# Performance work log

Measured on AMD Instinct MI355X. Metric: run time of the kernel, lower is better.

Reference implementation:

```python
import jax, jax.numpy as jnp
import numpy as np

N, IN_DIM, HID, HEADS, HOPS, NCLS, E = 20000, 1536, 256, 4, 3, 3, 320000
HD = HID // HEADS
EPS = 1e-5
NEG_SLOPE = 0.2


def layer_norm(x, g, b):
    mu = jnp.mean(x, axis=-1, keepdims=True)
    var = jnp.var(x, axis=-1, keepdims=True)
    return (x - mu) * jax.lax.rsqrt(var + EPS) * g + b


def gatv2(x, src, dst, Wl, bl, Wr, br, att, bias):
    # x: [N, HID]; src/dst: [E'] (self loops included)
    xl = (x @ Wl + bl).reshape(N, HEADS, HD)  # source transform
    xr = (x @ Wr + br).reshape(N, HEADS, HD)  # target transform
    e = jax.nn.leaky_relu(xl[src] + xr[dst], NEG_SLOPE)          # [E', H, D]
    logits = jnp.einsum('ehd,hd->eh', e, att)                     # [E', H]
    m = jax.ops.segment_max(logits, dst, num_segments=N)         # [N, H]
    ex = jnp.exp(logits - m[dst])
    denom = jax.ops.segment_sum(ex, dst, num_segments=N)
    alpha = ex / denom[dst]                                       # softmax per dst
    msg = xl[src] * alpha[:, :, None]                             # [E', H, D]
    out = jax.ops.segment_sum(msg, dst, num_segments=N)
    return out.reshape(N, HID) + bias


def setup_inputs() -> dict:
    key = jax.random.key(0)
    ks = jax.random.split(key, 20)
    s = lambda k, shp, sc: jax.random.normal(k, shp, jnp.float32) * sc
    return {
        'features': s(ks[0], (N, IN_DIM), 1.0),
        'edge_index': jax.random.randint(ks[1], (2, E), 0, N, jnp.int64),
        'proj_W': s(ks[2], (IN_DIM, HID), 0.02),
        'proj_b': jnp.zeros((HID,), jnp.float32),
        'n0_g': jnp.ones((HID,), jnp.float32),
        'n0_b': jnp.zeros((HID,), jnp.float32),
        'Wl': s(ks[3], (HOPS, HID, HID), 0.05),
        'bl': jnp.zeros((HOPS, HID), jnp.float32),
        'Wr': s(ks[4], (HOPS, HID, HID), 0.05),
        'br': jnp.zeros((HOPS, HID), jnp.float32),
        'att': s(ks[5], (HOPS, HEADS, HD), 0.1),
        'gbias': jnp.zeros((HOPS, HID), jnp.float32),
        'ln_g': jnp.ones((HOPS, HID), jnp.float32),
        'ln_b': jnp.zeros((HOPS, HID), jnp.float32),
        'h1_W': s(ks[6], (HID, HID), 0.05),
        'h1_b': jnp.zeros((HID,), jnp.float32),
        'h2_W': s(ks[7], (HID, NCLS), 0.05),
        'h2_b': jnp.zeros((NCLS,), jnp.float32),
    }


def reference(features, edge_index, proj_W, proj_b, n0_g, n0_b, Wl, bl, Wr, br,
              att, gbias, ln_g, ln_b, h1_W, h1_b, h2_W, h2_b):
    # add self loops (PyG GATv2Conv default)
    loop = jnp.arange(N, dtype=edge_index.dtype)
    src = jnp.concatenate([edge_index[0], loop])
    dst = jnp.concatenate([edge_index[1], loop])

    x = layer_norm(features @ proj_W + proj_b, n0_g, n0_b)
    for h in range(HOPS):
        g = gatv2(x, src, dst, Wl[h], bl[h], Wr[h], br[h], att[h], gbias[h])
        x = layer_norm(g + x, ln_g[h], ln_b[h])
    # head (dropout inactive at eval); torch GELU is exact erf form
    x = jax.nn.gelu(x @ h1_W + h1_b, approximate=False)
    return x @ h2_W + h2_b
```

## Files before the change

### kernel.cpp

```cpp
#include <hip/hip_runtime.h>
#include <hip/hip_bf16.h>
#include <math.h>

#define NN 20000
#define INDIM 1536
#define HID 256
#define NE 320000
#define NEDGE (NE + NN)
#define EPSV 1e-5f
#define NEG 0.2f

typedef unsigned short ushort_b;
typedef unsigned int uint32;
typedef __bf16 bf16x8 __attribute__((ext_vector_type(8)));
typedef float f32x4 __attribute__((ext_vector_type(4)));

#define AS1(p) ((const __attribute__((address_space(1))) void*)(p))
#define AS3(p) ((__attribute__((address_space(3))) void*)(p))

__device__ inline ushort_b f2bf(float x) {
  union { float f; uint32 u; } v; v.f = x;
  uint32 r = v.u + 0x7FFFu + ((v.u >> 16) & 1u);
  return (ushort_b)(r >> 16);
}
__device__ inline float bf2f(ushort_b h) {
  union { uint32 u; float f; } v; v.u = ((uint32)h) << 16;
  return v.f;
}
__device__ inline float4 ldbf4(const ushort_b* p) {
  ushort4 u = *(const ushort4*)p;
  float4 f;
  f.x = bf2f(u.x); f.y = bf2f(u.y); f.z = bf2f(u.z); f.w = bf2f(u.w);
  return f;
}

template<int OUTMODE>
__global__ __launch_bounds__(256, 3) void gemm_mfma(
    const float* __restrict__ Af,
    const ushort_b* __restrict__ Bt0, const ushort_b* __restrict__ Bt1,
    const float* __restrict__ bias0, const float* __restrict__ bias1,
    void* __restrict__ C0, void* __restrict__ C1,
    int Mstore, int Kloop, int Kstride, int kb0, int kb1)
{
  __shared__ ushort_b Bs[3 * 8192];
  const ushort_b* Bt = blockIdx.z ? Bt1 : Bt0;
  const float* bias  = blockIdx.z ? bias1 : bias0;
  void* Cv           = blockIdx.z ? C1 : C0;
  int kbase          = blockIdx.z ? kb1 : kb0;

  int tid = threadIdx.x;
  int wave = tid >> 6, lane = tid & 63;
  int quad = lane >> 4, mrow = lane & 15;
  int r0 = blockIdx.y * 64;
  int p  = blockIdx.x;
  int nk = Kloop >> 5;
  int nchunk = Kstride >> 5;
  int cb = kbase >> 5;

  int arow = r0 + (wave << 4) + mrow;
  if (arow >= Mstore) arow = Mstore - 1;
  const float* Aptr = Af + (size_t)arow * Kstride + kbase + (quad << 3);

  f32x4 acc[8] = {};
  float pA0[8], pA1[8];

  auto issueB = [&](int kc, int buf) {
    const char* g = (const char*)Bt + (((size_t)(p * nchunk + (cb + kc))) << 14);
    char* l = (char*)Bs + buf * 16384;
    int o = tid << 4;
#pragma unroll
    for (int pl = 0; pl < 2; pl++) {
      int off = (pl << 13) + o;
      __builtin_amdgcn_global_load_lds(AS1(g + off), AS3(l + off), 16, 0, 0);
      __builtin_amdgcn_global_load_lds(AS1(g + off + 4096), AS3(l + off + 4096), 16, 0, 0);
    }
  };
  auto loadA = [&](int k, float* dst) {
    const float* s = Aptr + (k << 5);
    *(float4*)(dst)     = *(const float4*)(s);
    *(float4*)(dst + 4) = *(const float4*)(s + 4);
  };
  auto cvtA = [&](const float* s, bf16x8& hh, bf16x8& ll) {
    union { bf16x8 v; uint32 u[4]; } H, L;
#pragma unroll
    for (int q2 = 0; q2 < 4; q2++) {
      float a = s[2 * q2], b = s[2 * q2 + 1];
      ushort_b h0 = f2bf(a), h1 = f2bf(b);
      H.u[q2] = (uint32)h0 | ((uint32)h1 << 16);
      L.u[q2] = (uint32)f2bf(a - bf2f(h0)) | ((uint32)f2bf(b - bf2f(h1)) << 16);
    }
    hh = H.v; ll = L.v;
  };
  auto computeStage = [&](int buf, const bf16x8& ah, const bf16x8& al) {
    const ushort_b* bp = Bs + buf * 8192;
#pragma unroll
    for (int u = 0; u < 8; u++) {
      bf16x8 bh = *(const bf16x8*)(bp + (u << 9) + (lane << 3));
      bf16x8 bl = *(const bf16x8*)(bp + 4096 + (u << 9) + (lane << 3));
      acc[u] = __builtin_amdgcn_mfma_f32_16x16x32_bf16(ah, bh, acc[u], 0, 0, 0);
      acc[u] = __builtin_amdgcn_mfma_f32_16x16x32_bf16(al, bh, acc[u], 0, 0, 0);
      acc[u] = __builtin_amdgcn_mfma_f32_16x16x32_bf16(ah, bl, acc[u], 0, 0, 0);
    }
  };

  loadA(0, pA0);
  issueB(0, 0);
  issueB(1, 1);
  loadA(1, pA1);
  asm volatile("s_waitcnt vmcnt(6)" ::: "memory");
  __builtin_amdgcn_sched_barrier(0);
  __builtin_amdgcn_s_barrier();
  __builtin_amdgcn_sched_barrier(0);

  int bcur = 0;
  for (int k = 0; k < nk; k += 2) {
    int b1 = bcur + 1; if (b1 >= 3) b1 -= 3;
    int b2 = bcur + 2; if (b2 >= 3) b2 -= 3;

    {
      bf16x8 ah, al;
      cvtA(pA0, ah, al);
      if (k + 2 < nk) { issueB(k + 2, b2); loadA(k + 2, pA0); }
      computeStage(bcur, ah, al);
      if (k + 2 < nk) { asm volatile("s_waitcnt vmcnt(6)" ::: "memory"); }
      else            { asm volatile("s_waitcnt vmcnt(2)" ::: "memory"); }
      __builtin_amdgcn_sched_barrier(0);
      __builtin_amdgcn_s_barrier();
      __builtin_amdgcn_sched_barrier(0);
    }
    {
      bf16x8 ah, al;
      cvtA(pA1, ah, al);
      if (k + 3 < nk) { issueB(k + 3, bcur); loadA(k + 3, pA1); }
      computeStage(b1, ah, al);
      if (k + 3 < nk) {
        asm volatile("s_waitcnt vmcnt(6)" ::: "memory");
        __builtin_amdgcn_sched_barrier(0);
        __builtin_amdgcn_s_barrier();
        __builtin_amdgcn_sched_barrier(0);
      }
    }
    bcur = b2;
  }

#pragma unroll
  for (int u = 0; u < 8; u++) {
    int col = (p << 7) + (u << 4) + mrow;
    float bb = bias[col];
#pragma unroll
    for (int r = 0; r < 4; r++) {
      int row = r0 + (wave << 4) + (quad << 2) + r;
      if (row < Mstore) {
        float v = acc[u][r] + bb;
        if (OUTMODE == 3) v = 0.5f * v * (1.f + erff(v * 0.70710678118654752f));
        if (OUTMODE == 2) ((ushort_b*)Cv)[(size_t)row * 256 + col] = f2bf(v);
        else              ((float*)Cv)[(size_t)row * 256 + col] = v;
      }
    }
  }
}

__device__ inline void prep_body(const float* __restrict__ W, int ldw, int nchunk,
                                 ushort_b* __restrict__ out, int c, int p, int tid)
{
  ushort_b* base = out + (((size_t)(p * nchunk + c)) << 13);
#pragma unroll
  for (int g0 = 0; g0 < 2; g0++) {
    int g = tid + (g0 << 8);
    int u = g >> 6, l = g & 63;
    int quad = l >> 4, mrow = l & 15;
    int col = (p << 7) + (u << 4) + mrow;
    int krow = (c << 5) + (quad << 3);
    uint32 hu[4], lu[4];
#pragma unroll
    for (int q2 = 0; q2 < 4; q2++) {
      float a = W[(size_t)(krow + 2 * q2) * ldw + col];
      float b = W[(size_t)(krow + 2 * q2 + 1) * ldw + col];
      ushort_b h0 = f2bf(a), h1 = f2bf(b);
      hu[q2] = (uint32)h0 | ((uint32)h1 << 16);
      lu[q2] = (uint32)f2bf(a - bf2f(h0)) | ((uint32)f2bf(b - bf2f(h1)) << 16);
    }
    *(uint4*)(base + (size_t)g * 8)        = make_uint4(hu[0], hu[1], hu[2], hu[3]);
    *(uint4*)(base + 4096 + (size_t)g * 8) = make_uint4(lu[0], lu[1], lu[2], lu[3]);
  }
}

__global__ __launch_bounds__(256) void prep_frag(
    const float* __restrict__ W, int ldw, int nchunk, ushort_b* __restrict__ out)
{
  prep_body(W, ldw, nchunk, out, blockIdx.x, blockIdx.y, threadIdx.x);
}

__global__ __launch_bounds__(256) void prep_frag7(
    const float* __restrict__ Wl, const float* __restrict__ Wr,
    const float* __restrict__ h1W, ushort_b* __restrict__ dst)
{
  int z = blockIdx.z;
  const float* W = (z < 3) ? Wl + (size_t)z * 65536
                 : (z < 6) ? Wr + (size_t)(z - 3) * 65536
                           : h1W;
  prep_body(W, 256, 8, dst + (size_t)z * 131072, blockIdx.x, blockIdx.y, threadIdx.x);
}

__global__ __launch_bounds__(256) void ln_sum_kernel(
    const float* __restrict__ in0, const float* __restrict__ in1,
    const float* __restrict__ g, const float* __restrict__ b,
    float* __restrict__ out, int n)
{
  int wave = threadIdx.x >> 6, lane = threadIdx.x & 63;
  int row = blockIdx.x * 4 + wave;
  if (row >= n) return;
  int c = lane << 2;
  float4 v = *(const float4*)(in0 + (size_t)row * HID + c);
  float4 v1 = *(const float4*)(in1 + (size_t)row * HID + c);
  v.x += v1.x; v.y += v1.y; v.z += v1.z; v.w += v1.w;
  float s1 = v.x + v.y + v.z + v.w;
  float s2 = v.x * v.x + v.y * v.y + v.z * v.z + v.w * v.w;
#pragma unroll
  for (int m = 1; m < 64; m <<= 1) {
    s1 += __shfl_xor(s1, m, 64);
    s2 += __shfl_xor(s2, m, 64);
  }
  float mu = s1 * (1.f / 256.f);
  float var = s2 * (1.f / 256.f) - mu * mu;
  float rstd = rsqrtf(var + EPSV);
  float4 gv = *(const float4*)(g + c);
  float4 bv = *(const float4*)(b + c);
  float4 o;
  o.x = (v.x - mu) * rstd * gv.x + bv.x;
  o.y = (v.y - mu) * rstd * gv.y + bv.y;
  o.z = (v.z - mu) * rstd * gv.z + bv.z;
  o.w = (v.w - mu) * rstd * gv.w + bv.w;
  *(float4*)(out + (size_t)row * HID + c) = o;
}

__global__ void count_kernel(const int* __restrict__ ei, int* __restrict__ cnt)
{
  int e = blockIdx.x * blockDim.x + threadIdx.x;
  if (e < NEDGE) {
    int d = (e < NE) ? ei[NE + e] : (e - NE);
    atomicAdd(&cnt[d], 1);
  }
}

__global__ __launch_bounds__(1024) void scan_kernel(
    const int* __restrict__ cnt, int* __restrict__ offs, int* __restrict__ cursor)
{
  __shared__ int sums[1024];
  int tid = threadIdx.x;
  const int CH = 20;
  int base = tid * CH;
  int loc[CH];
  int s = 0;
#pragma unroll
  for (int i = 0; i < CH; i++) {
    int idx = base + i;
    int v = (idx < NN) ? cnt[idx] : 0;
    loc[i] = s;
    s += v;
  }
  sums[tid] = s;
  __syncthreads();
  for (int off = 1; off < 1024; off <<= 1) {
    int t = (tid >= off) ? sums[tid - off] : 0;
    __syncthreads();
    sums[tid] += t;
    __syncthreads();
  }
  int pre = (tid == 0) ? 0 : sums[tid - 1];
#pragma unroll
  for (int i = 0; i < CH; i++) {
    int idx = base + i;
    if (idx < NN) { int e = pre + loc[i]; offs[idx] = e; cursor[idx] = e; }
  }
  if (tid == 0) offs[NN] = NEDGE;
}

__global__ void scatter_kernel(const int* __restrict__ ei, int* __restrict__ cursor,
                               int* __restrict__ csr_src)
{
  int e = blockIdx.x * blockDim.x + threadIdx.x;
  if (e < NEDGE) {
    int s, d;
    if (e < NE) { s = ei[e]; d = ei[NE + e]; }
    else { s = e - NE; d = e - NE; }
    int p = atomicAdd(&cursor[d], 1);
    csr_src[p] = s;
  }
}

__device__ inline float edge_logit(float4 xv, float4 xrv, float4 attv) {
  float e0 = xv.x + xrv.x, e1 = xv.y + xrv.y, e2 = xv.z + xrv.z, e3 = xv.w + xrv.w;
  e0 = (e0 > 0.f) ? e0 : NEG * e0;
  e1 = (e1 > 0.f) ? e1 : NEG * e1;
  e2 = (e2 > 0.f) ? e2 : NEG * e2;
  e3 = (e3 > 0.f) ? e3 : NEG * e3;
  float lc = e0 * attv.x + e1 * attv.y + e2 * attv.z + e3 * attv.w;
  lc += __shfl_xor(lc, 1, 16);
  lc += __shfl_xor(lc, 2, 16);
  lc += __shfl_xor(lc, 4, 16);
  lc += __shfl_xor(lc, 8, 16);
  return lc;
}

#define ACCUM(i, lg, xv) {                          \
    float w = __expf(lg);                            \
    lS[i] += w;                                      \
    pS##i##0 += w * xv.x; pS##i##1 += w * xv.y;      \
    pS##i##2 += w * xv.z; pS##i##3 += w * xv.w; }

__global__ __launch_bounds__(256) void gat_kernel(
    const ushort_b* __restrict__ xl, const ushort_b* __restrict__ xr,
    const float* __restrict__ x_in, const float* __restrict__ att,
    const float* __restrict__ gbias, const float* __restrict__ ln_g,
    const float* __restrict__ ln_b, const int* __restrict__ offs,
    const int* __restrict__ csr_src, float* __restrict__ x_out)
{
  __shared__ float gbuf[2][64][5];
  int wave = threadIdx.x >> 6, lane = threadIdx.x & 63;
  int nib = wave >> 1, sub = wave & 1;
  int node = blockIdx.x * 2 + nib;
  int c = lane << 2;
  float4 xrv = ldbf4(xr + (size_t)node * HID + c);
  float4 attv = *(const float4*)(att + c);

  float lS[4] = {0.f, 0.f, 0.f, 0.f};
  float pS00 = 0.f, pS01 = 0.f, pS02 = 0.f, pS03 = 0.f;
  float pS10 = 0.f, pS11 = 0.f, pS12 = 0.f, pS13 = 0.f;
  float pS20 = 0.f, pS21 = 0.f, pS22 = 0.f, pS23 = 0.f;
  float pS30 = 0.f, pS31 = 0.f, pS32 = 0.f, pS33 = 0.f;

  int beg = offs[node], end = offs[node + 1];
  int mid = beg + ((end - beg + 1) >> 1);
  int e  = sub ? mid : beg;
  int e1 = sub ? end : mid;
  for (; e + 3 < e1; e += 4) {
    int s0 = csr_src[e], s1 = csr_src[e + 1], s2 = csr_src[e + 2], s3 = csr_src[e + 3];
    float4 x0v = ldbf4(xl + (size_t)s0 * HID + c);
    float4 x1v = ldbf4(xl + (size_t)s1 * HID + c);
    float4 x2v = ldbf4(xl + (size_t)s2 * HID + c);
    float4 x3v = ldbf4(xl + (size_t)s3 * HID + c);
    float g0 = edge_logit(x0v, xrv, attv);
    float g1 = edge_logit(x1v, xrv, attv);
    float g2 = edge_logit(x2v, xrv, attv);
    float g3 = edge_logit(x3v, xrv, attv);
    ACCUM(0, g0, x0v);
    ACCUM(1, g1, x1v);
    ACCUM(2, g2, x2v);
    ACCUM(3, g3, x3v);
  }
  for (; e < e1; e++) {
    int s0 = csr_src[e];
    float4 x0v = ldbf4(xl + (size_t)s0 * HID + c);
    float g0 = edge_logit(x0v, xrv, attv);
    ACCUM(0, g0, x0v);
  }

  float l  = lS[0] + lS[1] + lS[2] + lS[3];
  float q0 = pS00 + pS10 + pS20 + pS30;
  float q1 = pS01 + pS11 + pS21 + pS31;
  float q2 = pS02 + pS12 + pS22 + pS32;
  float q3 = pS03 + pS13 + pS23 + pS33;

  if (sub) {
    gbuf[nib][lane][0] = l;
    gbuf[nib][lane][1] = q0;
    gbuf[nib][lane][2] = q1;
    gbuf[nib][lane][3] = q2;
    gbuf[nib][lane][4] = q3;
  }
  __syncthreads();
  if (sub) return;

  l  += gbuf[nib][lane][0];
  q0 += gbuf[nib][lane][1];
  q1 += gbuf[nib][lane][2];
  q2 += gbuf[nib][lane][3];
  q3 += gbuf[nib][lane][4];

  float inv = 1.f / l;
  float4 xv = *(const float4*)(x_in + (size_t)node * HID + c);
  float4 gb = *(const float4*)(gbias + c);
  float o0 = q0 * inv + gb.x + xv.x;
  float o1 = q1 * inv + gb.y + xv.y;
  float o2 = q2 * inv + gb.z + xv.z;
  float o3 = q3 * inv + gb.w + xv.w;
  float s1s = o0 + o1 + o2 + o3;
  float s2s = o0 * o0 + o1 * o1 + o2 * o2 + o3 * o3;
#pragma unroll
  for (int mmk = 1; mmk < 64; mmk <<= 1) {
    s1s += __shfl_xor(s1s, mmk, 64);
    s2s += __shfl_xor(s2s, mmk, 64);
  }
  float mu = s1s * (1.f / 256.f);
  float var = s2s * (1.f / 256.f) - mu * mu;
  float rstd = rsqrtf(var + EPSV);
  float4 gv = *(const float4*)(ln_g + c);
  float4 bv = *(const float4*)(ln_b + c);
  float4 o;
  o.x = (o0 - mu) * rstd * gv.x + bv.x;
  o.y = (o1 - mu) * rstd * gv.y + bv.y;
  o.z = (o2 - mu) * rstd * gv.z + bv.z;
  o.w = (o3 - mu) * rstd * gv.w + bv.w;
  *(float4*)(x_out + (size_t)node * HID + c) = o;
}

__global__ __launch_bounds__(256) void head2_kernel(
    const float* __restrict__ t1, const float* __restrict__ W,
    const float* __restrict__ bias, float* __restrict__ out)
{
  int wave = threadIdx.x >> 6, lane = threadIdx.x & 63;
  int row = blockIdx.x * 4 + wave;
  if (row >= NN) return;
  int c = lane << 2;
  float4 v = *(const float4*)(t1 + (size_t)row * HID + c);
  float p0 = 0.f, p1 = 0.f, p2 = 0.f;
#pragma unroll
  for (int j = 0; j < 4; j++) {
    float vj = (&v.x)[j];
    p0 += vj * W[(c + j) * 3 + 0];
    p1 += vj * W[(c + j) * 3 + 1];
    p2 += vj * W[(c + j) * 3 + 2];
  }
#pragma unroll
  for (int mm = 1; mm < 64; mm <<= 1) {
    p0 += __shfl_xor(p0, mm, 64);
    p1 += __shfl_xor(p1, mm, 64);
    p2 += __shfl_xor(p2, mm, 64);
  }
  if (lane == 0) {
    out[(size_t)row * 3 + 0] = p0 + bias[0];
    out[(size_t)row * 3 + 1] = p1 + bias[1];
    out[(size_t)row * 3 + 2] = p2 + bias[2];
  }
}

extern "C" void kernel_launch(void* const* d_in, const int* in_sizes, int n_in,
                              void* d_out, int out_size, void* d_ws, size_t ws_size,
                              hipStream_t stream)
{
  const float* features = (const float*)d_in[0];
  const int*   ei       = (const int*)d_in[1];
  const float* proj_W   = (const float*)d_in[2];
  const float* proj_b   = (const float*)d_in[3];
  const float* n0_g     = (const float*)d_in[4];
  const float* n0_b     = (const float*)d_in[5];
  const float* Wl       = (const float*)d_in[6];
  const float* bl       = (const float*)d_in[7];
  const float* Wr       = (const float*)d_in[8];
  const float* br       = (const float*)d_in[9];
  const float* att      = (const float*)d_in[10];
  const float* gbias    = (const float*)d_in[11];
  const float* ln_g     = (const float*)d_in[12];
  const float* ln_b     = (const float*)d_in[13];
  const float* h1_W     = (const float*)d_in[14];
  const float* h1_b     = (const float*)d_in[15];
  const float* h2_W     = (const float*)d_in[16];
  const float* h2_b     = (const float*)d_in[17];
  float* out = (float*)d_out;

  char* w = (char*)d_ws;
  float*    x0    = (float*)w;    w += (size_t)NN * HID * 4;
  float*    x1    = (float*)w;    w += (size_t)NN * HID * 4;
  float*    part1 = (float*)w;    w += (size_t)NN * HID * 4;
  ushort_b* xlb   = (ushort_b*)w; w += (size_t)NN * HID * 2;
  ushort_b* xrb   = (ushort_b*)w; w += (size_t)NN * HID * 2;
  ushort_b* wtp   = (ushort_b*)w; w += (size_t)2 * HID * INDIM * 2;
  ushort_b* w7    = (ushort_b*)w; w += (size_t)14 * HID * HID * 2;
  float* zbias = (float*)w; w += (size_t)HID * 4;
  int* cnt     = (int*)w;  w += (size_t)NN * 4;
  int* offs    = (int*)w;  w += (size_t)(NN + 1) * 4;
  int* cursor  = (int*)w;  w += (size_t)NN * 4;
  int* csr     = (int*)w;  w += (size_t)NEDGE * 4;

  hipMemsetAsync(cnt, 0, (size_t)NN * 4, stream);
  hipMemsetAsync(zbias, 0, (size_t)HID * 4, stream);
  count_kernel<<<(NEDGE + 255) / 256, 256, 0, stream>>>(ei, cnt);
  scan_kernel<<<1, 1024, 0, stream>>>(cnt, offs, cursor);
  scatter_kernel<<<(NEDGE + 255) / 256, 256, 0, stream>>>(ei, cursor, csr);

  prep_frag<<<dim3(INDIM / 32, 2), 256, 0, stream>>>(proj_W, HID, INDIM / 32, wtp);
  prep_frag7<<<dim3(8, 2, 7), 256, 0, stream>>>(Wl, Wr, h1_W, w7);

  const int MB = (NN + 63) / 64;
  dim3 gsplit(2, MB, 2);
  dim3 gsingle(2, MB, 1);

  gemm_mfma<0><<<gsplit, 256, 0, stream>>>(
      features, wtp, wtp, proj_b, zbias, x1, part1, NN, INDIM / 2, INDIM, 0, INDIM / 2);
  ln_sum_kernel<<<(NN + 3) / 4, 256, 0, stream>>>(x1, part1, n0_g, n0_b, x0, NN);

  float* xcur = x0;
  float* xnxt = x1;
  for (int h = 0; h < 3; h++) {
    gemm_mfma<2><<<gsplit, 256, 0, stream>>>(
        xcur, w7 + (size_t)h * 131072, w7 + (size_t)(3 + h) * 131072,
        bl + h * HID, br + h * HID, xlb, xrb, NN, HID, HID, 0, 0);
    gat_kernel<<<NN / 2, 256, 0, stream>>>(
        xlb, xrb, xcur, att + h * HID, gbias + h * HID,
        ln_g + h * HID, ln_b + h * HID, offs, csr, xnxt);
    float* t = xcur; xcur = xnxt; xnxt = t;
  }

  gemm_mfma<3><<<gsingle, 256, 0, stream>>>(
      xcur, w7 + (size_t)6 * 131072, w7 + (size_t)6 * 131072,
      h1_b, h1_b, part1, part1, NN, HID, HID, 0, 0);
  head2_kernel<<<(NN + 3) / 4, 256, 0, stream>>>(part1, h2_W, h2_b, out);
}
```

Measured before the change: 591.0 us.

## Double GEMM row tile per wave and use packed bf16 conversion

Each wave now computes two 16-row MFMA tiles instead of one, so the block covers 128 rows and each B fragment read from LDS is reused twice. The grid is halved to match, and the vmcnt waits are raised to account for the extra A loads. The fp32-to-bf16 hi/lo split now uses the v_cvt_pk_bf16_f32 instruction in place of manual rounding. The cost is more VGPRs for accumulators and A prefetch, which may lower occupancy under launch_bounds(256,3), and fewer blocks in the grid.

```diff
diff --git a/kernel.cpp b/kernel.cpp
--- a/kernel.cpp
+++ b/kernel.cpp
@@ -27,6 +27,14 @@
   union { uint32 u; float f; } v; v.u = ((uint32)h) << 16;
   return v.f;
 }
+__device__ inline float u2f(uint32 u) {
+  union { uint32 u; float f; } v; v.u = u; return v.f;
+}
+__device__ inline uint32 cvtpk_bf16(float a, float b) {
+  uint32 r;
+  asm("v_cvt_pk_bf16_f32 %0, %1, %2" : "=v"(r) : "v"(a), "v"(b));
+  return r;
+}
 __device__ inline float4 ldbf4(const ushort_b* p) {
   ushort4 u = *(const ushort4*)p;
   float4 f;
@@ -51,18 +59,21 @@
   int tid = threadIdx.x;
   int wave = tid >> 6, lane = tid & 63;
   int quad = lane >> 4, mrow = lane & 15;
-  int r0 = blockIdx.y * 64;
+  int r0 = blockIdx.y * 128;
   int p  = blockIdx.x;
   int nk = Kloop >> 5;
   int nchunk = Kstride >> 5;
   int cb = kbase >> 5;
 
-  int arow = r0 + (wave << 4) + mrow;
-  if (arow >= Mstore) arow = Mstore - 1;
-  const float* Aptr = Af + (size_t)arow * Kstride + kbase + (quad << 3);
-
-  f32x4 acc[8] = {};
-  float pA0[8], pA1[8];
+  int arow0 = r0 + (wave << 5) + mrow;
+  int arow1 = arow0 + 16;
+  if (arow0 >= Mstore) arow0 = Mstore - 1;
+  if (arow1 >= Mstore) arow1 = Mstore - 1;
+  const float* Aptr0 = Af + (size_t)arow0 * Kstride + kbase + (quad << 3);
+  const float* Aptr1 = Af + (size_t)arow1 * Kstride + kbase + (quad << 3);
+
+  f32x4 acc[2][8] = {};
+  float pA0[16], pA1[16];
 
   auto issueB = [&](int kc, int buf) {
     const char* g = (const char*)Bt + (((size_t)(p * nchunk + (cb + kc))) << 14);
@@ -76,30 +87,39 @@
     }
   };
   auto loadA = [&](int k, float* dst) {
-    const float* s = Aptr + (k << 5);
-    *(float4*)(dst)     = *(const float4*)(s);
-    *(float4*)(dst + 4) = *(const float4*)(s + 4);
+    const float* s0 = Aptr0 + (k << 5);
+    const float* s1 = Aptr1 + (k << 5);
+    *(float4*)(dst)      = *(const float4*)(s0);
+    *(float4*)(dst + 4)  = *(const float4*)(s0 + 4);
+    *(float4*)(dst + 8)  = *(const float4*)(s1);
+    *(float4*)(dst + 12) = *(const float4*)(s1 + 4);
   };
-  auto cvtA = [&](const float* s, bf16x8& hh, bf16x8& ll) {
+  auto cvtFrag = [&](const float* s, bf16x8& hh, bf16x8& ll) {
     union { bf16x8 v; uint32 u[4]; } H, L;
 #pragma unroll
     for (int q2 = 0; q2 < 4; q2++) {
       float a = s[2 * q2], b = s[2 * q2 + 1];
-      ushort_b h0 = f2bf(a), h1 = f2bf(b);
-      H.u[q2] = (uint32)h0 | ((uint32)h1 << 16);
-      L.u[q2] = (uint32)f2bf(a - bf2f(h0)) | ((uint32)f2bf(b - bf2f(h1)) << 16);
+      uint32 hp = cvtpk_bf16(a, b);
+      float fa = u2f(hp << 16);
+      float fb = u2f(hp & 0xffff0000u);
+      H.u[q2] = hp;
+      L.u[q2] = cvtpk_bf16(a - fa, b - fb);
     }
     hh = H.v; ll = L.v;
   };
-  auto computeStage = [&](int buf, const bf16x8& ah, const bf16x8& al) {
+  auto computeStage = [&](int buf, const bf16x8& ah0, const bf16x8& al0,
+                          const bf16x8& ah1, const bf16x8& al1) {
     const ushort_b* bp = Bs + buf * 8192;
 #pragma unroll
     for (int u = 0; u < 8; u++) {
       bf16x8 bh = *(const bf16x8*)(bp + (u << 9) + (lane << 3));
       bf16x8 bl = *(const bf16x8*)(bp + 4096 + (u << 9) + (lane << 3));
-      acc[u] = __builtin_amdgcn_mfma_f32_16x16x32_bf16(ah, bh, acc[u], 0, 0, 0);
-      acc[u] = __builtin_amdgcn_mfma_f32_16x16x32_bf16(al, bh, acc[u], 0, 0, 0);
-      acc[u] = __builtin_amdgcn_mfma_f32_16x16x32_bf16(ah, bl, acc[u], 0, 0, 0);
+      acc[0][u] = __builtin_amdgcn_mfma_f32_16x16x32_bf16(ah0, bh, acc[0][u], 0, 0, 0);
+      acc[0][u] = __builtin_amdgcn_mfma_f32_16x16x32_bf16(al0, bh, acc[0][u], 0, 0, 0);
+      acc[0][u] = __builtin_amdgcn_mfma_f32_16x16x32_bf16(ah0, bl, acc[0][u], 0, 0, 0);
+      acc[1][u] = __builtin_amdgcn_mfma_f32_16x16x32_bf16(ah1, bh, acc[1][u], 0, 0, 0);
+      acc[1][u] = __builtin_amdgcn_mfma_f32_16x16x32_bf16(al1, bh, acc[1][u], 0, 0, 0);
+      acc[1][u] = __builtin_amdgcn_mfma_f32_16x16x32_bf16(ah1, bl, acc[1][u], 0, 0, 0);
     }
   };
 
@@ -107,7 +127,7 @@
   issueB(0, 0);
   issueB(1, 1);
   loadA(1, pA1);
-  asm volatile("s_waitcnt vmcnt(6)" ::: "memory");
+  asm volatile("s_waitcnt vmcnt(8)" ::: "memory");
   __builtin_amdgcn_sched_barrier(0);
   __builtin_amdgcn_s_barrier();
   __builtin_amdgcn_sched_barrier(0);
@@ -118,23 +138,25 @@
     int b2 = bcur + 2; if (b2 >= 3) b2 -= 3;
 
     {
-      bf16x8 ah, al;
-      cvtA(pA0, ah, al);
+      bf16x8 ah0, al0, ah1, al1;
+      cvtFrag(pA0, ah0, al0);
+      cvtFrag(pA0 + 8, ah1, al1);
       if (k + 2 < nk) { issueB(k + 2, b2); loadA(k + 2, pA0); }
-      computeStage(bcur, ah, al);
-      if (k + 2 < nk) { asm volatile("s_waitcnt vmcnt(6)" ::: "memory"); }
-      else            { asm volatile("s_waitcnt vmcnt(2)" ::: "memory"); }
+      computeStage(bcur, ah0, al0, ah1, al1);
+      if (k + 2 < nk) { asm volatile("s_waitcnt vmcnt(8)" ::: "memory"); }
+      else            { asm volatile("s_waitcnt vmcnt(4)" ::: "memory"); }
       __builtin_amdgcn_sched_barrier(0);
       __builtin_amdgcn_s_barrier();
       __builtin_amdgcn_sched_barrier(0);
     }
     {
-      bf16x8 ah, al;
-      cvtA(pA1, ah, al);
+      bf16x8 ah0, al0, ah1, al1;
+      cvtFrag(pA1, ah0, al0);
+      cvtFrag(pA1 + 8, ah1, al1);
       if (k + 3 < nk) { issueB(k + 3, bcur); loadA(k + 3, pA1); }
-      computeStage(b1, ah, al);
+      computeStage(b1, ah0, al0, ah1, al1);
       if (k + 3 < nk) {
-        asm volatile("s_waitcnt vmcnt(6)" ::: "memory");
+        asm volatile("s_waitcnt vmcnt(8)" ::: "memory");
         __builtin_amdgcn_sched_barrier(0);
         __builtin_amdgcn_s_barrier();
         __builtin_amdgcn_sched_barrier(0);
@@ -148,13 +170,16 @@
     int col = (p << 7) + (u << 4) + mrow;
     float bb = bias[col];
 #pragma unroll
-    for (int r = 0; r < 4; r++) {
-      int row = r0 + (wave << 4) + (quad << 2) + r;
-      if (row < Mstore) {
-        float v = acc[u][r] + bb;
-        if (OUTMODE == 3) v = 0.5f * v * (1.f + erff(v * 0.70710678118654752f));
-        if (OUTMODE == 2) ((ushort_b*)Cv)[(size_t)row * 256 + col] = f2bf(v);
-        else              ((float*)Cv)[(size_t)row * 256 + col] = v;
+    for (int t = 0; t < 2; t++) {
+#pragma unroll
+      for (int r = 0; r < 4; r++) {
+        int row = r0 + (wave << 5) + (t << 4) + (quad << 2) + r;
+        if (row < Mstore) {
+          float v = acc[t][u][r] + bb;
+          if (OUTMODE == 3) v = 0.5f * v * (1.f + erff(v * 0.70710678118654752f));
+          if (OUTMODE == 2) ((ushort_b*)Cv)[(size_t)row * 256 + col] = f2bf(v);
+          else              ((float*)Cv)[(size_t)row * 256 + col] = v;
+        }
       }
     }
   }
@@ -482,7 +507,7 @@
   prep_frag<<<dim3(INDIM / 32, 2), 256, 0, stream>>>(proj_W, HID, INDIM / 32, wtp);
   prep_frag7<<<dim3(8, 2, 7), 256, 0, stream>>>(Wl, Wr, h1_W, w7);
 
-  const int MB = (NN + 63) / 64;
+  const int MB = (NN + 127) / 128;
   dim3 gsplit(2, MB, 2);
   dim3 gsingle(2, MB, 1);
 
```

New measurement: 586.0 us. No clear change (-0.8%).
